# Performance work log

Hardware: AMD Instinct MI355X
Metric: run time of the kernel (lower is better)

## Reference

```python
import jax, jax.numpy as jnp
import numpy as np

T, IN, BATCH = 512, 512, 256
HID, WID = 1024, 512


def setup_inputs() -> dict:
    key = jax.random.key(0)
    k_x, k_wh, k_bh, k_wy, k_by, k_h0 = jax.random.split(key, 6)
    s_h = 1.0 / np.sqrt(HID + IN)  # stabilise sigmoid pre-activations
    s_y = 1.0 / np.sqrt(HID)
    return {
        "xs": jax.random.normal(k_x, (T, IN, BATCH), dtype=jnp.float32),
        "W_h": jax.random.normal(k_wh, (HID, HID + IN), dtype=jnp.float32) * s_h,
        "b_h": jax.random.normal(k_bh, (HID, 1), dtype=jnp.float32) * 0.1,
        "W_y": jax.random.normal(k_wy, (WID, HID), dtype=jnp.float32) * s_y,
        "b_y": jax.random.normal(k_by, (WID, 1), dtype=jnp.float32) * 0.1,
        "h0": jax.random.normal(k_h0, (HID, 1), dtype=jnp.float32),
    }


def reference(xs, W_h, b_h, W_y, b_y, h0):
    # xs: [T, input_size, batch]; returns ys: [T, width, batch]
    batch = xs.shape[2]
    h_init = jnp.tile(h0, (1, batch))  # [HID, batch]

    def step(h, x):
        z = jnp.concatenate([h, x], axis=0)          # [HID+IN, batch]
        h_new = jax.nn.sigmoid(W_h @ z + b_h)        # [HID, batch]
        y = jax.nn.sigmoid(W_y @ h_new + b_y)        # [WID, batch]
        return h_new, y

    _, ys = jax.lax.scan(step, h_init, xs)
    return ys
```

## Files before the change

### kernel.cpp

```cpp
#include <hip/hip_runtime.h>
#include <hip/hip_bf16.h>

#define T_STEPS 512
#define INP     512
#define NB      256
#define HID     1024
#define WID     512
#define KZ      1536
#define ZSZ     (NB * KZ)

typedef short          bf16x8   __attribute__((ext_vector_type(8)));
typedef float          f32x4    __attribute__((ext_vector_type(4)));
typedef float          f32x2    __attribute__((ext_vector_type(2)));
typedef unsigned short ushort8  __attribute__((ext_vector_type(8)));
typedef unsigned short ushort2v __attribute__((ext_vector_type(2)));
typedef unsigned short ushort4v __attribute__((ext_vector_type(4)));
typedef unsigned       uint4v   __attribute__((ext_vector_type(4)));
typedef unsigned long long u64;

__device__ __forceinline__ unsigned short f2bf(float x) {
  __hip_bfloat16 h = __float2bfloat16(x);
  return __builtin_bit_cast(unsigned short, h);
}
__device__ __forceinline__ float sigm(float x) { return 1.0f / (1.0f + __expf(-x)); }

#define KEEP8(x) asm volatile("" : "+v"(x))

#define ZLOAD_FAST(dst, p) \
  asm volatile("global_load_dwordx4 %0, %1, off sc0" : "=v"(dst) : "v"(p))
#define ZLOAD_SLOW(dst, p) \
  asm volatile("global_load_dwordx4 %0, %1, off sc0 sc1" : "=v"(dst) : "v"(p))
#define ZWAIT() do { \
  asm volatile("s_waitcnt vmcnt(0)" ::: "memory"); \
  __builtin_amdgcn_sched_barrier(0); \
} while (0)

template <bool FAST>
__device__ __forceinline__ void zst4(unsigned short* p, ushort2v v) {
  if constexpr (FAST) *(unsigned*)p = __builtin_bit_cast(unsigned, v);
  else __hip_atomic_store((unsigned*)p, __builtin_bit_cast(unsigned, v),
                          __ATOMIC_RELAXED, __HIP_MEMORY_SCOPE_AGENT);
}
template <bool FAST>
__device__ __forceinline__ void zst8(unsigned short* p, ushort4v v) {
  if constexpr (FAST) *(u64*)p = __builtin_bit_cast(u64, v);
  else __hip_atomic_store((u64*)p, __builtin_bit_cast(u64, v),
                          __ATOMIC_RELAXED, __HIP_MEMORY_SCOPE_AGENT);
}

__device__ __forceinline__ void poll1(unsigned* p, unsigned tgt) {
  while (__hip_atomic_load(p, __ATOMIC_RELAXED, __HIP_MEMORY_SCOPE_AGENT) < tgt)
    __builtin_amdgcn_s_sleep(1);
}
__device__ __forceinline__ void pollh(unsigned* bar, unsigned ht, unsigned xt, unsigned yt) {
  uint4v v;
  for (;;) {
    asm volatile("global_load_dwordx4 %0, %1, off sc0 sc1\n\ts_waitcnt vmcnt(0)"
                 : "=v"(v) : "v"(bar) : "memory");
    if (v.x >= ht && v.y >= xt && v.z >= yt) return;
    __builtin_amdgcn_s_sleep(1);
  }
}
__device__ __forceinline__ void arrive(unsigned* ctr) {
  asm volatile("s_waitcnt vmcnt(0)" ::: "memory");
  __syncthreads();
  if (threadIdx.x == 0)
    __hip_atomic_fetch_add(ctr, 1u, __ATOMIC_RELAXED, __HIP_MEMORY_SCOPE_AGENT);
}

__global__ void elman_setup(const float* __restrict__ h0, const float* __restrict__ xs,
                            unsigned short* __restrict__ zT, unsigned* __restrict__ bars) {
  const int b = blockIdx.x;
  if (b == 0) {
    for (int j = threadIdx.x; j < 1024; j += blockDim.x) bars[j] = 0u;
  }
  for (int k = threadIdx.x; k < KZ; k += blockDim.x) {
    const float v = (k < HID) ? h0[k] : xs[(size_t)(k - HID) * NB + b];
    zT[(size_t)b * KZ + k] = f2bf(v);
  }
  for (int i = threadIdx.x; i < INP; i += blockDim.x)
    zT[(size_t)ZSZ + (size_t)b * KZ + HID + i] = f2bf(xs[(size_t)(INP + i) * NB + b]);
}

#define PSTR 36
#define PWSZ (32 * PSTR)

template <bool FAST>
__device__ __forceinline__ void run_phases(
    const float* __restrict__ xs,
    const float* __restrict__ Wh, const float* __restrict__ bh,
    const float* __restrict__ Wy, const float* __restrict__ by,
    unsigned short* __restrict__ zT, float* __restrict__ out,
    unsigned* line, float* P, int wg, int tid) {
  const int w = tid >> 6, lane = tid & 63;
  const int lr = lane & 15, lk = lane >> 4;

  if (wg < 128) {
    const int m0 = (wg >> 3) * 64;
    const int n0 = (wg & 7) * 32;
    const int kwh = w * 128;
    const int kwx = HID + w * 64;
    bf16x8 A[4][6];
#pragma unroll
    for (int mt = 0; mt < 4; ++mt)
#pragma unroll
      for (int kc = 0; kc < 6; ++kc) {
        const int kg = (kc < 4) ? (kwh + kc * 32) : (kwx + (kc - 4) * 32);
        const float* wp = Wh + (size_t)(m0 + mt * 16 + lr) * KZ + kg + lk * 8;
        const f32x4 f0 = *(const f32x4*)wp;
        const f32x4 f1 = *(const f32x4*)(wp + 4);
        ushort8 a;
#pragma unroll
        for (int e = 0; e < 4; ++e) { a[e] = f2bf(f0[e]); a[4 + e] = f2bf(f1[e]); }
        A[mt][kc] = __builtin_bit_cast(bf16x8, a);
      }
    const int lcol = tid >> 4;
    const int r2 = (tid & 15) * 2;
    f32x2 bias[2];
#pragma unroll
    for (int hf = 0; hf < 2; ++hf) bias[hf] = *(const f32x2*)&bh[m0 + hf * 32 + r2];
    float* Pw = P + w * (2 * PWSZ);

    for (int t = 0; t <= T_STEPS; ++t) {
#pragma unroll
      for (int mt = 0; mt < 4; ++mt)
#pragma unroll
        for (int kc = 0; kc < 6; ++kc) KEEP8(A[mt][kc]);
      if (t < T_STEPS) {
        const unsigned short* zc = zT + (size_t)(t & 3) * ZSZ;
        unsigned short* zn = zT + (size_t)((t + 1) & 3) * ZSZ;
        const unsigned short* zbh = zc + (size_t)(n0 + lr) * KZ + kwh + lk * 8;
        const unsigned short* zbx = zc + (size_t)(n0 + lr) * KZ + kwx + lk * 8;
        bf16x8 fx[2][2];
#pragma unroll
        for (int j = 0; j < 2; ++j)
#pragma unroll
          for (int nt = 0; nt < 2; ++nt) {
            if constexpr (FAST) ZLOAD_FAST(fx[j][nt], zbx + nt * (16 * KZ) + j * 32);
            else                ZLOAD_SLOW(fx[j][nt], zbx + nt * (16 * KZ) + j * 32);
          }
        ZWAIT();
        f32x4 acc[4][2];
#pragma unroll
        for (int mt = 0; mt < 4; ++mt)
#pragma unroll
          for (int nt = 0; nt < 2; ++nt) acc[mt][nt] = (f32x4){0.f, 0.f, 0.f, 0.f};
#pragma unroll
        for (int j = 0; j < 2; ++j)
#pragma unroll
          for (int nt = 0; nt < 2; ++nt)
#pragma unroll
            for (int mt = 0; mt < 4; ++mt)
              acc[mt][nt] = __builtin_amdgcn_mfma_f32_16x16x32_bf16(A[mt][4 + j], fx[j][nt], acc[mt][nt], 0, 0, 0);
        if (t >= 1) {
          if (tid == 0) pollh(line, 16u * (unsigned)t, 8u * (unsigned)(t - 1),
                              (t >= 2) ? 8u * (unsigned)(t - 2) : 0u);
          __syncthreads();
        }
        bf16x8 fh[4][2];
#pragma unroll
        for (int kc = 0; kc < 4; ++kc)
#pragma unroll
          for (int nt = 0; nt < 2; ++nt) {
            if constexpr (FAST) ZLOAD_FAST(fh[kc][nt], zbh + nt * (16 * KZ) + kc * 32);
            else                ZLOAD_SLOW(fh[kc][nt], zbh + nt * (16 * KZ) + kc * 32);
          }
        ZWAIT();
#pragma unroll
        for (int kc = 0; kc < 4; ++kc)
#pragma unroll
          for (int nt = 0; nt < 2; ++nt)
#pragma unroll
            for (int mt = 0; mt < 4; ++mt)
              acc[mt][nt] = __builtin_amdgcn_mfma_f32_16x16x32_bf16(A[mt][kc], fh[kc][nt], acc[mt][nt], 0, 0, 0);
#pragma unroll
        for (int hf = 0; hf < 2; ++hf)
#pragma unroll
          for (int mp = 0; mp < 2; ++mp)
#pragma unroll
            for (int nt = 0; nt < 2; ++nt)
              *(f32x4*)&Pw[hf * PWSZ + (nt * 16 + lr) * PSTR + mp * 16 + lk * 4] = acc[hf * 2 + mp][nt];
        __syncthreads();
#pragma unroll
        for (int hf = 0; hf < 2; ++hf) {
          f32x2 s = {0.f, 0.f};
#pragma unroll
          for (int ww = 0; ww < 8; ++ww)
            s += *(const f32x2*)&P[ww * (2 * PWSZ) + hf * PWSZ + lcol * PSTR + r2];
          s += bias[hf];
          ushort2v o2;
          o2[0] = f2bf(sigm(s[0]));
          o2[1] = f2bf(sigm(s[1]));
          zst4<FAST>(zn + (size_t)(n0 + lcol) * KZ + m0 + hf * 32 + r2, o2);
        }
      }
      arrive(line + 0);
    }

  } else if (wg < 192) {
    const int idx = wg - 128;
    const int m0 = (idx >> 3) * 64;
    const int n0 = (idx & 7) * 32;
    const int kw = w * 128;
    bf16x8 A[4][4];
#pragma unroll
    for (int mt = 0; mt < 4; ++mt)
#pragma unroll
      for (int kc = 0; kc < 4; ++kc) {
        const float* wp = Wy + (size_t)(m0 + mt * 16 + lr) * HID + kw + kc * 32 + lk * 8;
        const f32x4 f0 = *(const f32x4*)wp;
        const f32x4 f1 = *(const f32x4*)(wp + 4);
        ushort8 a;
#pragma unroll
        for (int e = 0; e < 4; ++e) { a[e] = f2bf(f0[e]); a[4 + e] = f2bf(f1[e]); }
        A[mt][kc] = __builtin_bit_cast(bf16x8, a);
      }
    const int lcol = tid & 31;
    const int r2 = (tid >> 5) * 2;
    f32x2 bias[2];
#pragma unroll
    for (int hf = 0; hf < 2; ++hf) bias[hf] = *(const f32x2*)&by[m0 + hf * 32 + r2];
    float* Pw = P + w * (2 * PWSZ);

    for (int t = 0; t <= T_STEPS; ++t) {
#pragma unroll
      for (int mt = 0; mt < 4; ++mt)
#pragma unroll
        for (int kc = 0; kc < 4; ++kc) KEEP8(A[mt][kc]);
      if (t >= 1) {
        const unsigned short* zc = zT + (size_t)(t & 3) * ZSZ;
        if (tid == 0) poll1(line + 0, 16u * (unsigned)t);
        __syncthreads();
        const unsigned short* zb = zc + (size_t)(n0 + lr) * KZ + kw + lk * 8;
        bf16x8 fb[4][2];
#pragma unroll
        for (int kc = 0; kc < 4; ++kc)
#pragma unroll
          for (int nt = 0; nt < 2; ++nt) {
            if constexpr (FAST) ZLOAD_FAST(fb[kc][nt], zb + nt * (16 * KZ) + kc * 32);
            else                ZLOAD_SLOW(fb[kc][nt], zb + nt * (16 * KZ) + kc * 32);
          }
        ZWAIT();
        f32x4 acc[4][2];
#pragma unroll
        for (int mt = 0; mt < 4; ++mt)
#pragma unroll
          for (int nt = 0; nt < 2; ++nt) acc[mt][nt] = (f32x4){0.f, 0.f, 0.f, 0.f};
#pragma unroll
        for (int kc = 0; kc < 4; ++kc)
#pragma unroll
          for (int nt = 0; nt < 2; ++nt)
#pragma unroll
            for (int mt = 0; mt < 4; ++mt)
              acc[mt][nt] = __builtin_amdgcn_mfma_f32_16x16x32_bf16(A[mt][kc], fb[kc][nt], acc[mt][nt], 0, 0, 0);
        float* op = out + (size_t)(t - 1) * (WID * NB);
#pragma unroll
        for (int hf = 0; hf < 2; ++hf)
#pragma unroll
          for (int mp = 0; mp < 2; ++mp)
#pragma unroll
            for (int nt = 0; nt < 2; ++nt)
              *(f32x4*)&Pw[hf * PWSZ + (nt * 16 + lr) * PSTR + mp * 16 + lk * 4] = acc[hf * 2 + mp][nt];
        __syncthreads();
#pragma unroll
        for (int hf = 0; hf < 2; ++hf) {
          f32x2 s = {0.f, 0.f};
#pragma unroll
          for (int ww = 0; ww < 8; ++ww)
            s += *(const f32x2*)&P[ww * (2 * PWSZ) + hf * PWSZ + lcol * PSTR + r2];
          s += bias[hf];
          const int row = m0 + hf * 32 + r2;
          op[(size_t)(row + 0) * NB + n0 + lcol] = sigm(s[0]);
          op[(size_t)(row + 1) * NB + n0 + lcol] = sigm(s[1]);
        }
      }
      arrive(line + 2);
    }

  } else {
    const int xi = wg - 192;
    const int i0 = (xi >> 3) * 64;
    const int b0 = (xi & 7) * 32;
    const int c = tid & 31, rb = tid >> 5;
    for (int t = 0; t <= T_STEPS; ++t) {
      if (t <= T_STEPS - 3) {
        unsigned short* zx = zT + (size_t)((t + 2) & 3) * ZSZ;
        const float* xp = xs + (size_t)(t + 2) * (INP * NB) + (size_t)(i0 + rb * 4) * NB + b0 + c;
        ushort4v o;
#pragma unroll
        for (int j = 0; j < 4; ++j) o[j] = f2bf(xp[(size_t)j * NB]);
        if (t >= 2 && tid == 0) poll1(line + 0, 16u * (unsigned)(t - 1));
        __syncthreads();
        zst8<FAST>(zx + (size_t)(b0 + c) * KZ + HID + i0 + rb * 4, o);
      }
      arrive(line + 1);
    }
  }
}

__global__ void __launch_bounds__(512, 2) elman_seq(
    const float* __restrict__ xs,
    const float* __restrict__ Wh, const float* __restrict__ bh,
    const float* __restrict__ Wy, const float* __restrict__ by,
    unsigned short* __restrict__ zT, float* __restrict__ out,
    unsigned* __restrict__ bars) {
  __shared__ float P[16 * PWSZ];
  __shared__ unsigned modeSh;
  const int wg = blockIdx.x, tid = threadIdx.x;
  unsigned* line = bars + (wg & 7) * 64;
  unsigned* xcds = bars + 512;
  unsigned* hbar = bars + 768;

  unsigned xcc;
  asm volatile("s_getreg_b32 %0, hwreg(HW_REG_XCC_ID)" : "=s"(xcc));
  if (tid == 0) {
    __hip_atomic_store(&xcds[wg], xcc + 1u, __ATOMIC_RELAXED, __HIP_MEMORY_SCOPE_AGENT);
    asm volatile("s_waitcnt vmcnt(0)" ::: "memory");
    __hip_atomic_fetch_add(hbar, 1u, __ATOMIC_RELAXED, __HIP_MEMORY_SCOPE_AGENT);
    while (__hip_atomic_load(hbar, __ATOMIC_RELAXED, __HIP_MEMORY_SCOPE_AGENT) < 256u)
      __builtin_amdgcn_s_sleep(1);
    const unsigned v0 = __hip_atomic_load(&xcds[wg & 7], __ATOMIC_RELAXED, __HIP_MEMORY_SCOPE_AGENT);
    unsigned m = 1u;
    for (int j = 1; j < 32; ++j)
      m &= (__hip_atomic_load(&xcds[(wg & 7) + 8 * j], __ATOMIC_RELAXED,
                              __HIP_MEMORY_SCOPE_AGENT) == v0) ? 1u : 0u;
    modeSh = m;
  }
  __syncthreads();

  if (modeSh)
    run_phases<true >(xs, Wh, bh, Wy, by, zT, out, line, P, wg, tid);
  else
    run_phases<false>(xs, Wh, bh, Wy, by, zT, out, line, P, wg, tid);
}

extern "C" void kernel_launch(void* const* d_in, const int* in_sizes, int n_in,
                              void* d_out, int out_size, void* d_ws, size_t ws_size,
                              hipStream_t stream) {
  (void)in_sizes; (void)n_in; (void)out_size; (void)ws_size;
  const float* xs  = (const float*)d_in[0];
  const float* W_h = (const float*)d_in[1];
  const float* b_h = (const float*)d_in[2];
  const float* W_y = (const float*)d_in[3];
  const float* b_y = (const float*)d_in[4];
  const float* h0  = (const float*)d_in[5];
  float* out = (float*)d_out;

  unsigned short* zT = (unsigned short*)d_ws;
  unsigned* bars = (unsigned*)(zT + 4 * (size_t)ZSZ);

  elman_setup<<<dim3(NB), dim3(256), 0, stream>>>(h0, xs, zT, bars);

  void* args[8];
  args[0] = (void*)&xs;  args[1] = (void*)&W_h; args[2] = (void*)&b_h;
  args[3] = (void*)&W_y; args[4] = (void*)&b_y; args[5] = (void*)&zT;
  args[6] = (void*)&out; args[7] = (void*)&bars;
  hipLaunchCooperativeKernel((void*)elman_seq, dim3(256), dim3(512), args, 0u, stream);
}
```

Measured before the change: 2.847 ms.

## Replace counter barriers with per-block flag slots and per-wave fine-grained gating

Each workgroup now stores its completed step number into its own slot instead of atomically incrementing a shared counter. Consumers poll only the producer slots they depend on: each wave of the hidden-state and output blocks waits only for the two h-producer blocks covering its K-slice. This removes the block-wide __syncthreads after polling and atomic contention on a single counter, letting waves start as soon as their inputs are ready. The register-pinning asm barriers on the weight fragments are also dropped, which may change register allocation. The risk is memory-ordering subtlety with relaxed stores and more polling traffic per wave.

```diff
diff --git a/kernel.cpp b/kernel.cpp
--- a/kernel.cpp
+++ b/kernel.cpp
@@ -24,8 +24,6 @@
 }
 __device__ __forceinline__ float sigm(float x) { return 1.0f / (1.0f + __expf(-x)); }
 
-#define KEEP8(x) asm volatile("" : "+v"(x))
-
 #define ZLOAD_FAST(dst, p) \
   asm volatile("global_load_dwordx4 %0, %1, off sc0" : "=v"(dst) : "v"(p))
 #define ZLOAD_SLOW(dst, p) \
@@ -48,24 +46,63 @@
                           __ATOMIC_RELAXED, __HIP_MEMORY_SCOPE_AGENT);
 }
 
-__device__ __forceinline__ void poll1(unsigned* p, unsigned tgt) {
-  while (__hip_atomic_load(p, __ATOMIC_RELAXED, __HIP_MEMORY_SCOPE_AGENT) < tgt)
-    __builtin_amdgcn_s_sleep(1);
-}
-__device__ __forceinline__ void pollh(unsigned* bar, unsigned ht, unsigned xt, unsigned yt) {
-  uint4v v;
-  for (;;) {
-    asm volatile("global_load_dwordx4 %0, %1, off sc0 sc1\n\ts_waitcnt vmcnt(0)"
-                 : "=v"(v) : "v"(bar) : "memory");
-    if (v.x >= ht && v.y >= xt && v.z >= yt) return;
-    __builtin_amdgcn_s_sleep(1);
-  }
-}
-__device__ __forceinline__ void arrive(unsigned* ctr) {
+#define SLD4(dst, p) \
+  asm volatile("global_load_dwordx4 %0, %1, off sc0 sc1" : "=v"(dst) : "v"(p))
+#define SLD1(dst, p) \
+  asm volatile("global_load_dword %0, %1, off sc0 sc1" : "=v"(dst) : "v"(p))
+#define SWAITM() asm volatile("s_waitcnt vmcnt(0)" ::: "memory")
+
+__device__ __forceinline__ void arrive_slot(unsigned* slot, unsigned val) {
   asm volatile("s_waitcnt vmcnt(0)" ::: "memory");
   __syncthreads();
   if (threadIdx.x == 0)
-    __hip_atomic_fetch_add(ctr, 1u, __ATOMIC_RELAXED, __HIP_MEMORY_SCOPE_AGENT);
+    __hip_atomic_store(slot, val, __ATOMIC_RELAXED, __HIP_MEMORY_SCOPE_AGENT);
+}
+__device__ __forceinline__ void gate_h(const unsigned* line, int w, unsigned t, unsigned yt) {
+  const unsigned* ph = line + ((w >> 1) << 2);
+  const unsigned* px = line + 16 + w;
+  for (;;) {
+    uint4v v; unsigned xv; uint4v y0, y1;
+    SLD4(v, ph);
+    SLD1(xv, px);
+    if (w == 0) { SLD4(y0, line + 24); SLD4(y1, line + 28); }
+    SWAITM();
+    const unsigned s0 = (w & 1) ? v.z : v.x;
+    const unsigned s1 = (w & 1) ? v.w : v.y;
+    bool ok = (s0 >= t) && (s1 >= t) && (xv >= t);
+    if (w == 0)
+      ok = ok && (y0.x >= yt) && (y0.y >= yt) && (y0.z >= yt) && (y0.w >= yt)
+              && (y1.x >= yt) && (y1.y >= yt) && (y1.z >= yt) && (y1.w >= yt);
+    if (ok) return;
+    __builtin_amdgcn_s_sleep(1);
+  }
+}
+__device__ __forceinline__ void gate_y(const unsigned* line, int w, unsigned t) {
+  const unsigned* ph = line + ((w >> 1) << 2);
+  for (;;) {
+    uint4v v;
+    SLD4(v, ph);
+    SWAITM();
+    const unsigned s0 = (w & 1) ? v.z : v.x;
+    const unsigned s1 = (w & 1) ? v.w : v.y;
+    if (s0 >= t && s1 >= t) return;
+    __builtin_amdgcn_s_sleep(1);
+  }
+}
+__device__ __forceinline__ void gate_x(const unsigned* line, unsigned t) {
+  for (;;) {
+    uint4v a, b, c, d;
+    SLD4(a, line);
+    SLD4(b, line + 4);
+    SLD4(c, line + 8);
+    SLD4(d, line + 12);
+    SWAITM();
+    if (a.x>=t && a.y>=t && a.z>=t && a.w>=t &&
+        b.x>=t && b.y>=t && b.z>=t && b.w>=t &&
+        c.x>=t && c.y>=t && c.z>=t && c.w>=t &&
+        d.x>=t && d.y>=t && d.z>=t && d.w>=t) return;
+    __builtin_amdgcn_s_sleep(1);
+  }
 }
 
 __global__ void elman_setup(const float* __restrict__ h0, const float* __restrict__ xs,
@@ -100,6 +137,7 @@
     const int n0 = (wg & 7) * 32;
     const int kwh = w * 128;
     const int kwx = HID + w * 64;
+    unsigned* slot = line + (wg >> 3);
     bf16x8 A[4][6];
 #pragma unroll
     for (int mt = 0; mt < 4; ++mt)
@@ -122,10 +160,6 @@
     float* Pw = P + w * (2 * PWSZ);
 
     for (int t = 0; t <= T_STEPS; ++t) {
-#pragma unroll
-      for (int mt = 0; mt < 4; ++mt)
-#pragma unroll
-        for (int kc = 0; kc < 6; ++kc) KEEP8(A[mt][kc]);
       if (t < T_STEPS) {
         const unsigned short* zc = zT + (size_t)(t & 3) * ZSZ;
         unsigned short* zn = zT + (size_t)((t + 1) & 3) * ZSZ;
@@ -152,11 +186,8 @@
 #pragma unroll
             for (int mt = 0; mt < 4; ++mt)
               acc[mt][nt] = __builtin_amdgcn_mfma_f32_16x16x32_bf16(A[mt][4 + j], fx[j][nt], acc[mt][nt], 0, 0, 0);
-        if (t >= 1) {
-          if (tid == 0) pollh(line, 16u * (unsigned)t, 8u * (unsigned)(t - 1),
-                              (t >= 2) ? 8u * (unsigned)(t - 2) : 0u);
-          __syncthreads();
-        }
+        if (t >= 1 && lane == 0)
+          gate_h(line, w, (unsigned)t, (t >= 3) ? (unsigned)(t - 2) : 0u);
         bf16x8 fh[4][2];
 #pragma unroll
         for (int kc = 0; kc < 4; ++kc)
@@ -194,7 +225,7 @@
           zst4<FAST>(zn + (size_t)(n0 + lcol) * KZ + m0 + hf * 32 + r2, o2);
         }
       }
-      arrive(line + 0);
+      arrive_slot(slot, (unsigned)(t + 1));
     }
 
   } else if (wg < 192) {
@@ -202,6 +233,7 @@
     const int m0 = (idx >> 3) * 64;
     const int n0 = (idx & 7) * 32;
     const int kw = w * 128;
+    unsigned* slot = line + 24 + (idx >> 3);
     bf16x8 A[4][4];
 #pragma unroll
     for (int mt = 0; mt < 4; ++mt)
@@ -223,14 +255,9 @@
     float* Pw = P + w * (2 * PWSZ);
 
     for (int t = 0; t <= T_STEPS; ++t) {
-#pragma unroll
-      for (int mt = 0; mt < 4; ++mt)
-#pragma unroll
-        for (int kc = 0; kc < 4; ++kc) KEEP8(A[mt][kc]);
       if (t >= 1) {
         const unsigned short* zc = zT + (size_t)(t & 3) * ZSZ;
-        if (tid == 0) poll1(line + 0, 16u * (unsigned)t);
-        __syncthreads();
+        if (lane == 0) gate_y(line, w, (unsigned)t);
         const unsigned short* zb = zc + (size_t)(n0 + lr) * KZ + kw + lk * 8;
         bf16x8 fb[4][2];
 #pragma unroll
@@ -274,7 +301,7 @@
           op[(size_t)(row + 1) * NB + n0 + lcol] = sigm(s[1]);
         }
       }
-      arrive(line + 2);
+      arrive_slot(slot, (unsigned)(t + 1));
     }
 
   } else {
@@ -282,6 +309,7 @@
     const int i0 = (xi >> 3) * 64;
     const int b0 = (xi & 7) * 32;
     const int c = tid & 31, rb = tid >> 5;
+    unsigned* slot = line + 16 + (xi >> 3);
     for (int t = 0; t <= T_STEPS; ++t) {
       if (t <= T_STEPS - 3) {
         unsigned short* zx = zT + (size_t)((t + 2) & 3) * ZSZ;
@@ -289,11 +317,11 @@
         ushort4v o;
 #pragma unroll
         for (int j = 0; j < 4; ++j) o[j] = f2bf(xp[(size_t)j * NB]);
-        if (t >= 2 && tid == 0) poll1(line + 0, 16u * (unsigned)(t - 1));
+        if (t >= 2 && tid == 0) gate_x(line, (unsigned)(t - 1));
         __syncthreads();
         zst8<FAST>(zx + (size_t)(b0 + c) * KZ + HID + i0 + rb * 4, o);
       }
-      arrive(line + 1);
+      arrive_slot(slot, (unsigned)(t + 1));
     }
   }
 }
```

Measured after the change: 4.217 ms. +48.1%, slower.

## Deepen z ring to six slots and pipeline z loads against MFMAs

Applied to the files above, without the earlier changes.

Grows the z staging ring from four to six buffers so the x-producer blocks can run three steps ahead, which relaxes the cross-block wait conditions. The recurrent blocks now split K uniformly per wave (192 columns each, mixing h and x) and issue all z loads after the barrier, then overlap them with MFMAs using staged vmcnt waits. The output blocks use the same staged waits. The KEEP8 register pinning is removed, and the workspace grows by two z buffers. The goal is to hide load latency on the serial critical path, at the cost of now loading the x part after the poll rather than before it.

```diff
diff --git a/kernel.cpp b/kernel.cpp
--- a/kernel.cpp
+++ b/kernel.cpp
@@ -8,6 +8,7 @@
 #define WID     512
 #define KZ      1536
 #define ZSZ     (NB * KZ)
+#define ZR      6
 
 typedef short          bf16x8   __attribute__((ext_vector_type(8)));
 typedef float          f32x4    __attribute__((ext_vector_type(4)));
@@ -24,14 +25,12 @@
 }
 __device__ __forceinline__ float sigm(float x) { return 1.0f / (1.0f + __expf(-x)); }
 
-#define KEEP8(x) asm volatile("" : "+v"(x))
-
 #define ZLOAD_FAST(dst, p) \
   asm volatile("global_load_dwordx4 %0, %1, off sc0" : "=v"(dst) : "v"(p))
 #define ZLOAD_SLOW(dst, p) \
   asm volatile("global_load_dwordx4 %0, %1, off sc0 sc1" : "=v"(dst) : "v"(p))
-#define ZWAIT() do { \
-  asm volatile("s_waitcnt vmcnt(0)" ::: "memory"); \
+#define ZWAITN(n) do { \
+  asm volatile("s_waitcnt vmcnt(" #n ")" ::: "memory"); \
   __builtin_amdgcn_sched_barrier(0); \
 } while (0)
 
@@ -78,8 +77,10 @@
     const float v = (k < HID) ? h0[k] : xs[(size_t)(k - HID) * NB + b];
     zT[(size_t)b * KZ + k] = f2bf(v);
   }
-  for (int i = threadIdx.x; i < INP; i += blockDim.x)
-    zT[(size_t)ZSZ + (size_t)b * KZ + HID + i] = f2bf(xs[(size_t)(INP + i) * NB + b]);
+  for (int i = threadIdx.x; i < INP; i += blockDim.x) {
+    zT[(size_t)ZSZ     + (size_t)b * KZ + HID + i] = f2bf(xs[(size_t)(INP     + i) * NB + b]);
+    zT[(size_t)2 * ZSZ + (size_t)b * KZ + HID + i] = f2bf(xs[(size_t)(2 * INP + i) * NB + b]);
+  }
 }
 
 #define PSTR 36
@@ -98,15 +99,13 @@
   if (wg < 128) {
     const int m0 = (wg >> 3) * 64;
     const int n0 = (wg & 7) * 32;
-    const int kwh = w * 128;
-    const int kwx = HID + w * 64;
+    const int kw = w * 192;
     bf16x8 A[4][6];
 #pragma unroll
     for (int mt = 0; mt < 4; ++mt)
 #pragma unroll
       for (int kc = 0; kc < 6; ++kc) {
-        const int kg = (kc < 4) ? (kwh + kc * 32) : (kwx + (kc - 4) * 32);
-        const float* wp = Wh + (size_t)(m0 + mt * 16 + lr) * KZ + kg + lk * 8;
+        const float* wp = Wh + (size_t)(m0 + mt * 16 + lr) * KZ + kw + kc * 32 + lk * 8;
         const f32x4 f0 = *(const f32x4*)wp;
         const f32x4 f1 = *(const f32x4*)(wp + 4);
         ushort8 a;
@@ -122,57 +121,53 @@
     float* Pw = P + w * (2 * PWSZ);
 
     for (int t = 0; t <= T_STEPS; ++t) {
-#pragma unroll
-      for (int mt = 0; mt < 4; ++mt)
-#pragma unroll
-        for (int kc = 0; kc < 6; ++kc) KEEP8(A[mt][kc]);
       if (t < T_STEPS) {
-        const unsigned short* zc = zT + (size_t)(t & 3) * ZSZ;
-        unsigned short* zn = zT + (size_t)((t + 1) & 3) * ZSZ;
-        const unsigned short* zbh = zc + (size_t)(n0 + lr) * KZ + kwh + lk * 8;
-        const unsigned short* zbx = zc + (size_t)(n0 + lr) * KZ + kwx + lk * 8;
-        bf16x8 fx[2][2];
-#pragma unroll
-        for (int j = 0; j < 2; ++j)
-#pragma unroll
-          for (int nt = 0; nt < 2; ++nt) {
-            if constexpr (FAST) ZLOAD_FAST(fx[j][nt], zbx + nt * (16 * KZ) + j * 32);
-            else                ZLOAD_SLOW(fx[j][nt], zbx + nt * (16 * KZ) + j * 32);
-          }
-        ZWAIT();
-        f32x4 acc[4][2];
-#pragma unroll
-        for (int mt = 0; mt < 4; ++mt)
-#pragma unroll
-          for (int nt = 0; nt < 2; ++nt) acc[mt][nt] = (f32x4){0.f, 0.f, 0.f, 0.f};
-#pragma unroll
-        for (int j = 0; j < 2; ++j)
-#pragma unroll
-          for (int nt = 0; nt < 2; ++nt)
-#pragma unroll
-            for (int mt = 0; mt < 4; ++mt)
-              acc[mt][nt] = __builtin_amdgcn_mfma_f32_16x16x32_bf16(A[mt][4 + j], fx[j][nt], acc[mt][nt], 0, 0, 0);
+        const unsigned short* zc = zT + (size_t)(t % ZR) * ZSZ;
+        unsigned short* zn = zT + (size_t)((t + 1) % ZR) * ZSZ;
         if (t >= 1) {
-          if (tid == 0) pollh(line, 16u * (unsigned)t, 8u * (unsigned)(t - 1),
-                              (t >= 2) ? 8u * (unsigned)(t - 2) : 0u);
+          if (tid == 0) pollh(line, 16u * (unsigned)t,
+                              (t >= 3) ? 8u * (unsigned)(t - 2) : 0u,
+                              (t >= 5) ? 8u * (unsigned)(t - 4) : 0u);
           __syncthreads();
         }
-        bf16x8 fh[4][2];
-#pragma unroll
-        for (int kc = 0; kc < 4; ++kc)
+        const unsigned short* zb = zc + (size_t)(n0 + lr) * KZ + kw + lk * 8;
+        bf16x8 bfr[6][2];
+#pragma unroll
+        for (int kc = 0; kc < 6; ++kc)
 #pragma unroll
           for (int nt = 0; nt < 2; ++nt) {
-            if constexpr (FAST) ZLOAD_FAST(fh[kc][nt], zbh + nt * (16 * KZ) + kc * 32);
-            else                ZLOAD_SLOW(fh[kc][nt], zbh + nt * (16 * KZ) + kc * 32);
+            if constexpr (FAST) ZLOAD_FAST(bfr[kc][nt], zb + nt * (16 * KZ) + kc * 32);
+            else                ZLOAD_SLOW(bfr[kc][nt], zb + nt * (16 * KZ) + kc * 32);
           }
-        ZWAIT();
-#pragma unroll
-        for (int kc = 0; kc < 4; ++kc)
-#pragma unroll
-          for (int nt = 0; nt < 2; ++nt)
-#pragma unroll
-            for (int mt = 0; mt < 4; ++mt)
-              acc[mt][nt] = __builtin_amdgcn_mfma_f32_16x16x32_bf16(A[mt][kc], fh[kc][nt], acc[mt][nt], 0, 0, 0);
+        f32x4 acc[4][2];
+#pragma unroll
+        for (int mt = 0; mt < 4; ++mt)
+#pragma unroll
+          for (int nt = 0; nt < 2; ++nt) acc[mt][nt] = (f32x4){0.f, 0.f, 0.f, 0.f};
+        ZWAITN(8);
+#pragma unroll
+        for (int kc = 0; kc < 2; ++kc)
+#pragma unroll
+          for (int nt = 0; nt < 2; ++nt)
+#pragma unroll
+            for (int mt = 0; mt < 4; ++mt)
+              acc[mt][nt] = __builtin_amdgcn_mfma_f32_16x16x32_bf16(A[mt][kc], bfr[kc][nt], acc[mt][nt], 0, 0, 0);
+        ZWAITN(4);
+#pragma unroll
+        for (int kc = 2; kc < 4; ++kc)
+#pragma unroll
+          for (int nt = 0; nt < 2; ++nt)
+#pragma unroll
+            for (int mt = 0; mt < 4; ++mt)
+              acc[mt][nt] = __builtin_amdgcn_mfma_f32_16x16x32_bf16(A[mt][kc], bfr[kc][nt], acc[mt][nt], 0, 0, 0);
+        ZWAITN(0);
+#pragma unroll
+        for (int kc = 4; kc < 6; ++kc)
+#pragma unroll
+          for (int nt = 0; nt < 2; ++nt)
+#pragma unroll
+            for (int mt = 0; mt < 4; ++mt)
+              acc[mt][nt] = __builtin_amdgcn_mfma_f32_16x16x32_bf16(A[mt][kc], bfr[kc][nt], acc[mt][nt], 0, 0, 0);
 #pragma unroll
         for (int hf = 0; hf < 2; ++hf)
 #pragma unroll
@@ -223,12 +218,8 @@
     float* Pw = P + w * (2 * PWSZ);
 
     for (int t = 0; t <= T_STEPS; ++t) {
-#pragma unroll
-      for (int mt = 0; mt < 4; ++mt)
-#pragma unroll
-        for (int kc = 0; kc < 4; ++kc) KEEP8(A[mt][kc]);
       if (t >= 1) {
-        const unsigned short* zc = zT + (size_t)(t & 3) * ZSZ;
+        const unsigned short* zc = zT + (size_t)(t % ZR) * ZSZ;
         if (tid == 0) poll1(line + 0, 16u * (unsigned)t);
         __syncthreads();
         const unsigned short* zb = zc + (size_t)(n0 + lr) * KZ + kw + lk * 8;
@@ -240,14 +231,22 @@
             if constexpr (FAST) ZLOAD_FAST(fb[kc][nt], zb + nt * (16 * KZ) + kc * 32);
             else                ZLOAD_SLOW(fb[kc][nt], zb + nt * (16 * KZ) + kc * 32);
           }
-        ZWAIT();
         f32x4 acc[4][2];
 #pragma unroll
         for (int mt = 0; mt < 4; ++mt)
 #pragma unroll
           for (int nt = 0; nt < 2; ++nt) acc[mt][nt] = (f32x4){0.f, 0.f, 0.f, 0.f};
-#pragma unroll
-        for (int kc = 0; kc < 4; ++kc)
+        ZWAITN(4);
+#pragma unroll
+        for (int kc = 0; kc < 2; ++kc)
+#pragma unroll
+          for (int nt = 0; nt < 2; ++nt)
+#pragma unroll
+            for (int mt = 0; mt < 4; ++mt)
+              acc[mt][nt] = __builtin_amdgcn_mfma_f32_16x16x32_bf16(A[mt][kc], fb[kc][nt], acc[mt][nt], 0, 0, 0);
+        ZWAITN(0);
+#pragma unroll
+        for (int kc = 2; kc < 4; ++kc)
 #pragma unroll
           for (int nt = 0; nt < 2; ++nt)
 #pragma unroll
@@ -283,13 +282,13 @@
     const int b0 = (xi & 7) * 32;
     const int c = tid & 31, rb = tid >> 5;
     for (int t = 0; t <= T_STEPS; ++t) {
-      if (t <= T_STEPS - 3) {
-        unsigned short* zx = zT + (size_t)((t + 2) & 3) * ZSZ;
-        const float* xp = xs + (size_t)(t + 2) * (INP * NB) + (size_t)(i0 + rb * 4) * NB + b0 + c;
+      if (t <= T_STEPS - 4) {
+        unsigned short* zx = zT + (size_t)((t + 3) % ZR) * ZSZ;
+        const float* xp = xs + (size_t)(t + 3) * (INP * NB) + (size_t)(i0 + rb * 4) * NB + b0 + c;
         ushort4v o;
 #pragma unroll
         for (int j = 0; j < 4; ++j) o[j] = f2bf(xp[(size_t)j * NB]);
-        if (t >= 2 && tid == 0) poll1(line + 0, 16u * (unsigned)(t - 1));
+        if (t >= 3 && tid == 0) poll1(line + 0, 16u * (unsigned)(t - 2));
         __syncthreads();
         zst8<FAST>(zx + (size_t)(b0 + c) * KZ + HID + i0 + rb * 4, o);
       }
@@ -347,7 +346,7 @@
   float* out = (float*)d_out;
 
   unsigned short* zT = (unsigned short*)d_ws;
-  unsigned* bars = (unsigned*)(zT + 4 * (size_t)ZSZ);
+  unsigned* bars = (unsigned*)(zT + (size_t)ZR * ZSZ);
 
   elman_setup<<<dim3(NB), dim3(256), 0, stream>>>(h0, xs, zT, bars);
 
```

New measurement: 2.608 ms. -8.4%, faster.
